# Kernel optimization log

Measured on AMD Instinct MI355X. Metric: run time of the kernel, lower is better.

## Reference

```python
import jax, jax.numpy as jnp
import numpy as np

SEQ_LEN = 4096
NUM_EIGH = 40
D_IN = 64
D_OUT = 64
K_U = 3
BSZ = 2


def _spectral_filters(L, K):
    # Hankel matrix Z_ij = 2/((i+j)^3 - (i+j)), i,j in [1, L]
    e = np.arange(1, L + 1, dtype=np.float64)
    s = e[:, None] + e[None, :]
    Z = 2.0 / (s ** 3 - s)
    sigma, phi = np.linalg.eigh(Z)
    phi_k = phi[:, -K:] * sigma[-K:] ** 0.25  # (L, K)
    return jnp.asarray(phi_k, dtype=jnp.float32)


def setup_inputs() -> dict:
    key = jax.random.key(0)
    kx, km, kp, kn = jax.random.split(key, 4)
    x = jax.random.normal(kx, (BSZ, SEQ_LEN, D_IN), dtype=jnp.float32)
    phi = _spectral_filters(SEQ_LEN, NUM_EIGH)  # (L, K)
    M = jax.random.normal(km, (D_OUT, D_IN, K_U), dtype=jnp.float32) / D_IN
    M_phi_plus = jax.random.normal(kp, (NUM_EIGH, D_IN, D_OUT), dtype=jnp.float32) / 10.0
    M_phi_minus = jax.random.normal(kn, (NUM_EIGH, D_IN, D_OUT), dtype=jnp.float32) / 10.0
    return {"x": x, "phi": phi, "M": M, "M_phi_plus": M_phi_plus, "M_phi_minus": M_phi_minus}


def _stu_forward(x, phi, M, M_phi_plus, M_phi_minus):
    bsz, L, d_in = x.shape
    n = int(2 ** np.ceil(np.log2(2 * L - 1)))  # FFT length (8192)
    t = jnp.arange(L)
    sgn = jnp.where(t % 2 == 1, -1.0, 1.0).astype(x.dtype)  # (L,)

    # FFT of [u, u*sgn] once over d_in (K-expansion deferred to freq domain; FFT is linear)
    U = jnp.stack([x, x * sgn[None, :, None]], axis=-1)        # (b, L, d, 2)
    U_f = jnp.fft.rfft(U, n=n, axis=1)                         # (b, nf, d, 2)
    v_f = jnp.fft.rfft(phi.astype(jnp.float32), n=n, axis=0)   # (nf, K)

    prod = v_f[None, :, :, None, None] * U_f[:, :, None, :, :]  # (b, nf, K, d, 2)
    U_conv = jnp.fft.irfft(prod, n=n, axis=1)[:, :L]            # (b, L, K, d, 2)
    U_plus = U_conv[..., 0]
    U_minus = U_conv[..., 1] * sgn[None, :, None, None]

    # spectral tensordot: contract (K, d_in) -> d_out
    spec = (jnp.einsum('blkd,kdo->blo', U_plus, M_phi_plus)
            + jnp.einsum('blkd,kdo->blo', U_minus, M_phi_minus))

    ar = jnp.zeros((bsz, L, M.shape[0]), dtype=x.dtype)
    for i in range(M.shape[2]):  # k_u is small and fixed
        y_i = jnp.einsum('bli,oi->blo', x, M[:, :, i])
        if i > 0:
            y_i = jnp.pad(y_i[:, : L - i], ((0, 0), (i, 0), (0, 0)))
        ar = ar + y_i
    return spec + ar


def reference(x, phi, M, M_phi_plus, M_phi_minus):
    return _stu_forward(x, phi, M, M_phi_plus, M_phi_minus)
```

## Files before the change

kernel.cpp:

```cpp
#include <hip/hip_runtime.h>

typedef short bf16x8 __attribute__((ext_vector_type(8)));
typedef float f32x4 __attribute__((ext_vector_type(4)));
typedef unsigned short u16;

__device__ __forceinline__ u16 f2bf(float f) {
    unsigned u = __builtin_bit_cast(unsigned, f);
    return (u16)((u + 0x7fffu + ((u >> 16) & 1u)) >> 16);
}

__global__ void k_prep(const float* __restrict__ x, u16* __restrict__ xpad,
                       const float* __restrict__ Mp, const float* __restrict__ Mm,
                       float* __restrict__ ApT, float* __restrict__ AmT,
                       float* __restrict__ out, int* __restrict__ counter) {
    __shared__ float tp[64 * 65], tm[64 * 65];
    if (blockIdx.x < 1024) {
        int gid = blockIdx.x * 256 + threadIdx.x;
        int b   = gid >> 17;
        int rem = gid & 131071;
        int r   = rem >> 4;
        int c4  = rem & 15;
        u16 o0 = 0, o1 = 0, o2 = 0, o3 = 0;
        if (r >= 4096) {
            const f32x4 v = *(const f32x4*)(x + ((b << 12) + (r - 4096)) * 64 + c4 * 4);
            o0 = f2bf(v.x); o1 = f2bf(v.y); o2 = f2bf(v.z); o3 = f2bf(v.w);
        }
        u16* p = xpad + ((b << 13) + r) * 64 + c4 * 4;
        p[0] = o0; p[1] = o1; p[2] = o2; p[3] = o3;
    } else if (blockIdx.x < 1064) {
        const int k = blockIdx.x - 1024, tid = threadIdx.x;
        for (int f = tid; f < 4096; f += 256) {
            int d = f >> 6, o = f & 63;
            float p = Mp[k * 4096 + f], m = Mm[k * 4096 + f];
            tp[o * 65 + d] = p + m;
            tm[o * 65 + d] = p - m;
        }
        __syncthreads();
        for (int f = tid; f < 4096; f += 256) {
            int o = f >> 6, d = f & 63;
            ApT[k * 4096 + f] = tp[o * 65 + d];
            AmT[k * 4096 + f] = tm[o * 65 + d];
        }
    } else {
        const int bz = blockIdx.x - 1064;
        if (bz == 0 && threadIdx.x == 0) *counter = 0;
        float* po = out + bz * 4096;
        #pragma unroll
        for (int i = 0; i < 4; ++i)
            *(f32x4*)(po + (threadIdx.x + i * 256) * 4) = (f32x4){0.f, 0.f, 0.f, 0.f};
    }
}

__global__ __launch_bounds__(256)
void k_build_w(const float* __restrict__ phi, const float* __restrict__ ApT,
               const float* __restrict__ AmT, const float* __restrict__ Mar,
               u16* __restrict__ wg) {
    const int sb = blockIdx.x;
    const int qb = blockIdx.y;
    const int s0 = sb * 64;
    const int q  = qb * 256 + threadIdx.x;
    const int o  = q >> 6, d = q & 63;

    float ap[40], am[40];
    #pragma unroll
    for (int k = 0; k < 40; ++k) { ap[k] = ApT[k * 4096 + q]; am[k] = AmT[k * 4096 + q]; }

    for (int j = 0; j < 64; j += 2) {
        const float* ph = phi + (s0 + j) * 40;
        float a0 = 0.f, a1 = 0.f, b0 = 0.f, b1 = 0.f;
        #pragma unroll
        for (int k = 0; k < 40; k += 2) { a0 += ph[k] * ap[k]; a1 += ph[k + 1] * ap[k + 1]; }
        #pragma unroll
        for (int k = 0; k < 40; k += 2) { b0 += ph[40 + k] * am[k]; b1 += ph[41 + k] * am[k + 1]; }
        float ev = a0 + a1, ov = b0 + b1;
        int s = s0 + j;
        if (s < 3)     ev += Mar[o * 192 + d * 3 + s];
        if (s + 1 < 3) ov += Mar[o * 192 + d * 3 + s + 1];
        wg[(size_t)s * 4096 + q]       = f2bf(ev);
        wg[(size_t)(s + 1) * 4096 + q] = f2bf(ov);
    }
}

__global__ __launch_bounds__(256, 2)
void k_spectral(const u16* __restrict__ xpad, const u16* __restrict__ wg,
                float* __restrict__ out, int* __restrict__ counter) {
    __shared__ __align__(16) u16 xs[2 * 191 * 64];
    __shared__ __align__(16) u16 wsm[2 * 64 * 64];
    __shared__ int sh;

    const int tid  = threadIdx.x;
    const int lane = tid & 63, w = tid >> 6;
    const int m15  = lane & 15, q4 = lane >> 4;
    const int par  = w >> 1, batch = w & 1;
    const int f0 = tid * 2, f1 = tid * 2 + 1;
    const int l0 = (((f0 >> 3) * 8) + ((f0 & 7) ^ ((f0 >> 3) & 7))) * 8;
    const int l1 = (((f1 >> 3) * 8) + ((f1 & 7) ^ ((f1 >> 3) & 7))) * 8;

    for (;;) {
        __syncthreads();
        if (tid == 0) sh = atomicAdd(counter, 1);
        __syncthreads();
        const int U = sh;
        if (U >= 1120) break;

        int mu = U, shalf = 0, slen = 64;
        if (U >= 992) { mu = 992 + ((U - 992) >> 1); shalf = (U - 992) & 1; slen = 32; }
        int g = 0;
        #pragma unroll 1
        while (g < 31 && (g + 1) * (64 - g) <= mu) ++g;
        const int rem = mu - g * (65 - g);
        const int cnt = 32 - g;
        const int col = (rem >= cnt) ? 1 : 0;
        const int J = 2 * g + col;
        const int I = g + (col ? rem - cnt : rem);
        const int t0 = I << 7, s0 = (J << 6) + (shalf << 5);
        const int nrows = 127 + slen;
        const int jmax = slen >> 1;
        const int base = 4096 + t0 - s0 - (slen - 1);

        const u16* wbase = wg + (size_t)s0 * 4096;
        bf16x8 pre[4];
        pre[0] = *(const bf16x8*)(wbase + f0 * 8);
        pre[1] = *(const bf16x8*)(wbase + f1 * 8);
        pre[2] = *(const bf16x8*)(wbase + 4096 + f0 * 8);
        pre[3] = *(const bf16x8*)(wbase + 4096 + f1 * 8);

        #pragma unroll
        for (int b = 0; b < 2; ++b) {
            #pragma unroll 1
            for (int f = tid; f < nrows * 8; f += 256) {
                int r = f >> 3, c = f & 7;
                bf16x8 v = *(const bf16x8*)(xpad + (size_t)((b << 13) + base + r) * 64 + c * 8);
                *(bf16x8*)(xs + ((b * 191 + r) * 8 + (c ^ (r & 7))) * 8) = v;
            }
        }

        f32x4 acc[8][4];
        #pragma unroll
        for (int mt = 0; mt < 8; ++mt)
            #pragma unroll
            for (int nt = 0; nt < 4; ++nt)
                acc[mt][nt] = (f32x4){0.f, 0.f, 0.f, 0.f};

        const u16* xb = xs + batch * (191 * 64);
        const u16* wpar = wsm + par * 4096;

        #pragma unroll 1
        for (int j = 0; j < jmax; ++j) {
            __syncthreads();
            *(bf16x8*)(wsm + l0)        = pre[0];
            *(bf16x8*)(wsm + l1)        = pre[1];
            *(bf16x8*)(wsm + 4096 + l0) = pre[2];
            *(bf16x8*)(wsm + 4096 + l1) = pre[3];
            __syncthreads();
            if (j < jmax - 1) {
                const u16* wp = wbase + (size_t)(2 * j + 2) * 4096;
                pre[0] = *(const bf16x8*)(wp + f0 * 8);
                pre[1] = *(const bf16x8*)(wp + f1 * 8);
                pre[2] = *(const bf16x8*)(wp + 4096 + f0 * 8);
                pre[3] = *(const bf16x8*)(wp + 4096 + f1 * 8);
            }
            const int ds = 2 * j + par;
            #pragma unroll
            for (int ks = 0; ks < 2; ++ks) {
                const int kq = ks * 4 + q4;
                bf16x8 bf[4];
                #pragma unroll
                for (int nt = 0; nt < 4; ++nt) {
                    int o = nt * 16 + m15;
                    bf[nt] = *(const bf16x8*)(wpar + (o * 8 + (kq ^ (o & 7))) * 8);
                }
                #pragma unroll
                for (int mt = 0; mt < 8; ++mt) {
                    int r = mt * 16 + m15 + (slen - 1) - ds;
                    bf16x8 av = *(const bf16x8*)(xb + (r * 8 + (kq ^ (r & 7))) * 8);
                    #pragma unroll
                    for (int nt = 0; nt < 4; ++nt)
                        acc[mt][nt] = __builtin_amdgcn_mfma_f32_16x16x32_bf16(
                            av, bf[nt], acc[mt][nt], 0, 0, 0);
                }
            }
        }

        float* fs = (float*)wsm;
        #pragma unroll
        for (int rd = 0; rd < 4; ++rd) {
            __syncthreads();
            if (par == 1) {
                #pragma unroll
                for (int i = 0; i < 8; ++i) {
                    int ti = rd * 8 + i;
                    *(f32x4*)(fs + (batch * 8 + i) * 256 + lane * 4) = acc[ti >> 2][ti & 3];
                }
            }
            __syncthreads();
            if (par == 0) {
                #pragma unroll
                for (int i = 0; i < 8; ++i) {
                    int ti = rd * 8 + i;
                    f32x4 v = *(const f32x4*)(fs + (batch * 8 + i) * 256 + lane * 4);
                    acc[ti >> 2][ti & 3] += v;
                }
            }
        }

        if (par == 0) {
            #pragma unroll
            for (int mt = 0; mt < 8; ++mt) {
                int t = t0 + mt * 16 + q4 * 4;
                #pragma unroll
                for (int nt = 0; nt < 4; ++nt) {
                    int o = nt * 16 + m15;
                    float* op = out + (size_t)((batch << 12) + t) * 64 + o;
                    #pragma unroll
                    for (int r = 0; r < 4; ++r)
                        atomicAdd(op + r * 64, acc[mt][nt][r]);
                }
            }
        }
    }
}

extern "C" void kernel_launch(void* const* d_in, const int* in_sizes, int n_in,
                              void* d_out, int out_size, void* d_ws, size_t ws_size,
                              hipStream_t stream) {
    const float* x   = (const float*)d_in[0];
    const float* phi = (const float*)d_in[1];
    const float* M   = (const float*)d_in[2];
    const float* Mp  = (const float*)d_in[3];
    const float* Mm  = (const float*)d_in[4];
    float* out = (float*)d_out;

    int* counter = (int*)d_ws;
    u16* xpad = (u16*)((char*)d_ws + 4096);
    u16* wg   = (u16*)((char*)d_ws + 4096 + 2097152);
    float* ApT = (float*)((char*)d_ws + 4096 + 2097152 + 33554432);
    float* AmT = ApT + 40 * 4096;

    k_prep<<<1192, 256, 0, stream>>>(x, xpad, Mp, Mm, ApT, AmT, out, counter);
    k_build_w<<<dim3(64, 16), 256, 0, stream>>>(phi, ApT, AmT, M, wg);
    k_spectral<<<512, 256, 0, stream>>>(xpad, wg, out, counter);
}
```

Before: 236.8 us.

## Restructure spectral MFMA loop to reuse A fragments across shifted filter tiles

The spectral kernel's inner loop is restructured. Warps now split the 64-wide d_in contraction into halves (khalf) instead of splitting the shift parity. Each iteration loads 4 (or 2) weight tiles spaced 16 shifts apart into enlarged shared memory, and the A fragments from the x rows are loaded into registers once and reused across those tiles via a sliding register window. This cuts repeated LDS reads of x and halves the number of barrier-separated iterations. In exchange it uses more LDS and registers, which could pressure occupancy under launch_bounds(256,2).

```diff
diff --git a/kernel.cpp b/kernel.cpp
--- a/kernel.cpp
+++ b/kernel.cpp
@@ -81,17 +81,79 @@
     }
 }
 
+
+template<int SLEN>
+__device__ __forceinline__ void run_tiles(const u16* __restrict__ wg,
+                                          const u16* xb, u16* wsm,
+                                          int s0, int kq, int m15,
+                                          int l0, int l1, int f0, int f1,
+                                          f32x4 (&acc)[8][4]) {
+    constexpr int G = SLEN / 16;
+    bf16x8 pre[G][2];
+    #pragma unroll
+    for (int t = 0; t < G; ++t) {
+        const u16* wp = wg + (size_t)(s0 + 16 * t) * 4096;
+        pre[t][0] = *(const bf16x8*)(wp + f0 * 8);
+        pre[t][1] = *(const bf16x8*)(wp + f1 * 8);
+    }
+    #pragma unroll 1
+    for (int dl = 0; dl < 16; ++dl) {
+        __syncthreads();
+        #pragma unroll
+        for (int t = 0; t < G; ++t) {
+            *(bf16x8*)(wsm + t * 4096 + l0) = pre[t][0];
+            *(bf16x8*)(wsm + t * 4096 + l1) = pre[t][1];
+        }
+        bf16x8 af[8 + G - 1];
+        const int rbase = m15 + (SLEN - 1) - dl;
+        #pragma unroll
+        for (int sg = 0; sg < 8; ++sg) {
+            int r = rbase + 16 * sg;
+            af[(G - 1) + sg] = *(const bf16x8*)(xb + (r * 8 + (kq ^ (r & 7))) * 8);
+        }
+        __syncthreads();
+        if (dl < 15) {
+            #pragma unroll
+            for (int t = 0; t < G; ++t) {
+                const u16* wp = wg + (size_t)(s0 + dl + 1 + 16 * t) * 4096;
+                pre[t][0] = *(const bf16x8*)(wp + f0 * 8);
+                pre[t][1] = *(const bf16x8*)(wp + f1 * 8);
+            }
+        }
+        #pragma unroll
+        for (int g = 0; g < G; ++g) {
+            if (g > 0) {
+                int r = rbase - 16 * g;
+                af[(G - 1) - g] = *(const bf16x8*)(xb + (r * 8 + (kq ^ (r & 7))) * 8);
+            }
+            bf16x8 bf[4];
+            #pragma unroll
+            for (int nt = 0; nt < 4; ++nt) {
+                int o = nt * 16 + m15;
+                bf[nt] = *(const bf16x8*)(wsm + g * 4096 + (o * 8 + (kq ^ (o & 7))) * 8);
+            }
+            #pragma unroll
+            for (int mt = 0; mt < 8; ++mt)
+                #pragma unroll
+                for (int nt = 0; nt < 4; ++nt)
+                    acc[mt][nt] = __builtin_amdgcn_mfma_f32_16x16x32_bf16(
+                        af[(G - 1) + mt - g], bf[nt], acc[mt][nt], 0, 0, 0);
+        }
+    }
+}
+
 __global__ __launch_bounds__(256, 2)
 void k_spectral(const u16* __restrict__ xpad, const u16* __restrict__ wg,
                 float* __restrict__ out, int* __restrict__ counter) {
     __shared__ __align__(16) u16 xs[2 * 191 * 64];
-    __shared__ __align__(16) u16 wsm[2 * 64 * 64];
+    __shared__ __align__(16) u16 wsm[4 * 64 * 64];
     __shared__ int sh;
 
     const int tid  = threadIdx.x;
     const int lane = tid & 63, w = tid >> 6;
     const int m15  = lane & 15, q4 = lane >> 4;
-    const int par  = w >> 1, batch = w & 1;
+    const int khalf = w >> 1, batch = w & 1;
+    const int kq = khalf * 4 + q4;
     const int f0 = tid * 2, f1 = tid * 2 + 1;
     const int l0 = (((f0 >> 3) * 8) + ((f0 & 7) ^ ((f0 >> 3) & 7))) * 8;
     const int l1 = (((f1 >> 3) * 8) + ((f1 & 7) ^ ((f1 >> 3) & 7))) * 8;
@@ -115,15 +177,7 @@
         const int I = g + (col ? rem - cnt : rem);
         const int t0 = I << 7, s0 = (J << 6) + (shalf << 5);
         const int nrows = 127 + slen;
-        const int jmax = slen >> 1;
         const int base = 4096 + t0 - s0 - (slen - 1);
-
-        const u16* wbase = wg + (size_t)s0 * 4096;
-        bf16x8 pre[4];
-        pre[0] = *(const bf16x8*)(wbase + f0 * 8);
-        pre[1] = *(const bf16x8*)(wbase + f1 * 8);
-        pre[2] = *(const bf16x8*)(wbase + 4096 + f0 * 8);
-        pre[3] = *(const bf16x8*)(wbase + 4096 + f1 * 8);
 
         #pragma unroll
         for (int b = 0; b < 2; ++b) {
@@ -143,50 +197,17 @@
                 acc[mt][nt] = (f32x4){0.f, 0.f, 0.f, 0.f};
 
         const u16* xb = xs + batch * (191 * 64);
-        const u16* wpar = wsm + par * 4096;
-
-        #pragma unroll 1
-        for (int j = 0; j < jmax; ++j) {
-            __syncthreads();
-            *(bf16x8*)(wsm + l0)        = pre[0];
-            *(bf16x8*)(wsm + l1)        = pre[1];
-            *(bf16x8*)(wsm + 4096 + l0) = pre[2];
-            *(bf16x8*)(wsm + 4096 + l1) = pre[3];
-            __syncthreads();
-            if (j < jmax - 1) {
-                const u16* wp = wbase + (size_t)(2 * j + 2) * 4096;
-                pre[0] = *(const bf16x8*)(wp + f0 * 8);
-                pre[1] = *(const bf16x8*)(wp + f1 * 8);
-                pre[2] = *(const bf16x8*)(wp + 4096 + f0 * 8);
-                pre[3] = *(const bf16x8*)(wp + 4096 + f1 * 8);
-            }
-            const int ds = 2 * j + par;
-            #pragma unroll
-            for (int ks = 0; ks < 2; ++ks) {
-                const int kq = ks * 4 + q4;
-                bf16x8 bf[4];
-                #pragma unroll
-                for (int nt = 0; nt < 4; ++nt) {
-                    int o = nt * 16 + m15;
-                    bf[nt] = *(const bf16x8*)(wpar + (o * 8 + (kq ^ (o & 7))) * 8);
-                }
-                #pragma unroll
-                for (int mt = 0; mt < 8; ++mt) {
-                    int r = mt * 16 + m15 + (slen - 1) - ds;
-                    bf16x8 av = *(const bf16x8*)(xb + (r * 8 + (kq ^ (r & 7))) * 8);
-                    #pragma unroll
-                    for (int nt = 0; nt < 4; ++nt)
-                        acc[mt][nt] = __builtin_amdgcn_mfma_f32_16x16x32_bf16(
-                            av, bf[nt], acc[mt][nt], 0, 0, 0);
-                }
-            }
-        }
+
+        if (slen == 64)
+            run_tiles<64>(wg, xb, wsm, s0, kq, m15, l0, l1, f0, f1, acc);
+        else
+            run_tiles<32>(wg, xb, wsm, s0, kq, m15, l0, l1, f0, f1, acc);
 
         float* fs = (float*)wsm;
         #pragma unroll
         for (int rd = 0; rd < 4; ++rd) {
             __syncthreads();
-            if (par == 1) {
+            if (khalf == 1) {
                 #pragma unroll
                 for (int i = 0; i < 8; ++i) {
                     int ti = rd * 8 + i;
@@ -194,7 +215,7 @@
                 }
             }
             __syncthreads();
-            if (par == 0) {
+            if (khalf == 0) {
                 #pragma unroll
                 for (int i = 0; i < 8; ++i) {
                     int ti = rd * 8 + i;
@@ -204,7 +225,7 @@
             }
         }
 
-        if (par == 0) {
+        if (khalf == 0) {
             #pragma unroll
             for (int mt = 0; mt < 8; ++mt) {
                 int t = t0 + mt * 16 + q4 * 4;
```

Result: slower. 255.5 us (+7.9%).

## Fuse prep and weight-build kernels, double-buffer spectral weight tiles

Applied to the files above, without the earlier changes.

Merges the prep and filter-weight build kernels into one launch. The build blocks now compute (Mp±Mm) directly from the original layout instead of going through an intermediate transposed buffer, and stage phi rows in shared memory for vectorized reads. In the spectral kernel the weight tile in LDS is double-buffered, which removes one barrier per iteration. This raises LDS use per block, and the untransposed loads of Mp/Mm are strided, so they coalesce poorly.

```diff
diff --git a/kernel.cpp b/kernel.cpp
--- a/kernel.cpp
+++ b/kernel.cpp
@@ -9,11 +9,13 @@
     return (u16)((u + 0x7fffu + ((u >> 16) & 1u)) >> 16);
 }
 
-__global__ void k_prep(const float* __restrict__ x, u16* __restrict__ xpad,
-                       const float* __restrict__ Mp, const float* __restrict__ Mm,
-                       float* __restrict__ ApT, float* __restrict__ AmT,
-                       float* __restrict__ out, int* __restrict__ counter) {
-    __shared__ float tp[64 * 65], tm[64 * 65];
+__global__ __launch_bounds__(256)
+void k_prepbuild(const float* __restrict__ x, u16* __restrict__ xpad,
+                 const float* __restrict__ phi,
+                 const float* __restrict__ Mp, const float* __restrict__ Mm,
+                 const float* __restrict__ Mar, u16* __restrict__ wg,
+                 float* __restrict__ out, int* __restrict__ counter) {
+    __shared__ __align__(16) float phis[32 * 40];
     if (blockIdx.x < 1024) {
         int gid = blockIdx.x * 256 + threadIdx.x;
         int b   = gid >> 17;
@@ -27,57 +29,47 @@
         }
         u16* p = xpad + ((b << 13) + r) * 64 + c4 * 4;
         p[0] = o0; p[1] = o1; p[2] = o2; p[3] = o3;
-    } else if (blockIdx.x < 1064) {
-        const int k = blockIdx.x - 1024, tid = threadIdx.x;
-        for (int f = tid; f < 4096; f += 256) {
-            int d = f >> 6, o = f & 63;
-            float p = Mp[k * 4096 + f], m = Mm[k * 4096 + f];
-            tp[o * 65 + d] = p + m;
-            tm[o * 65 + d] = p - m;
-        }
-        __syncthreads();
-        for (int f = tid; f < 4096; f += 256) {
-            int o = f >> 6, d = f & 63;
-            ApT[k * 4096 + f] = tp[o * 65 + d];
-            AmT[k * 4096 + f] = tm[o * 65 + d];
-        }
-    } else {
-        const int bz = blockIdx.x - 1064;
+    } else if (blockIdx.x < 1152) {
+        const int bz = blockIdx.x - 1024;
         if (bz == 0 && threadIdx.x == 0) *counter = 0;
         float* po = out + bz * 4096;
         #pragma unroll
         for (int i = 0; i < 4; ++i)
             *(f32x4*)(po + (threadIdx.x + i * 256) * 4) = (f32x4){0.f, 0.f, 0.f, 0.f};
-    }
-}
-
-__global__ __launch_bounds__(256)
-void k_build_w(const float* __restrict__ phi, const float* __restrict__ ApT,
-               const float* __restrict__ AmT, const float* __restrict__ Mar,
-               u16* __restrict__ wg) {
-    const int sb = blockIdx.x;
-    const int qb = blockIdx.y;
-    const int s0 = sb * 64;
-    const int q  = qb * 256 + threadIdx.x;
-    const int o  = q >> 6, d = q & 63;
-
-    float ap[40], am[40];
-    #pragma unroll
-    for (int k = 0; k < 40; ++k) { ap[k] = ApT[k * 4096 + q]; am[k] = AmT[k * 4096 + q]; }
-
-    for (int j = 0; j < 64; j += 2) {
-        const float* ph = phi + (s0 + j) * 40;
-        float a0 = 0.f, a1 = 0.f, b0 = 0.f, b1 = 0.f;
-        #pragma unroll
-        for (int k = 0; k < 40; k += 2) { a0 += ph[k] * ap[k]; a1 += ph[k + 1] * ap[k + 1]; }
-        #pragma unroll
-        for (int k = 0; k < 40; k += 2) { b0 += ph[40 + k] * am[k]; b1 += ph[41 + k] * am[k + 1]; }
-        float ev = a0 + a1, ov = b0 + b1;
-        int s = s0 + j;
-        if (s < 3)     ev += Mar[o * 192 + d * 3 + s];
-        if (s + 1 < 3) ov += Mar[o * 192 + d * 3 + s + 1];
-        wg[(size_t)s * 4096 + q]       = f2bf(ev);
-        wg[(size_t)(s + 1) * 4096 + q] = f2bf(ov);
+    } else {
+        const int bi = blockIdx.x - 1152;
+        const int sb = bi >> 4, qb = bi & 15;
+        const int s0 = sb * 32;
+        const int q  = qb * 256 + threadIdx.x;
+        const int o  = q >> 6, d = q & 63;
+
+        for (int f = threadIdx.x; f < 1280; f += 256) phis[f] = phi[s0 * 40 + f];
+
+        float ap[40], am[40];
+        #pragma unroll
+        for (int k = 0; k < 40; ++k) {
+            float p = Mp[k * 4096 + d * 64 + o];
+            float m = Mm[k * 4096 + d * 64 + o];
+            ap[k] = p + m; am[k] = p - m;
+        }
+        __syncthreads();
+
+        for (int j = 0; j < 32; j += 2) {
+            const float* ph = phis + j * 40;
+            float ev = 0.f, ov = 0.f;
+            #pragma unroll
+            for (int k = 0; k < 40; k += 4) {
+                f32x4 p0 = *(const f32x4*)(ph + k);
+                f32x4 p1 = *(const f32x4*)(ph + 40 + k);
+                ev += p0.x * ap[k] + p0.y * ap[k + 1] + p0.z * ap[k + 2] + p0.w * ap[k + 3];
+                ov += p1.x * am[k] + p1.y * am[k + 1] + p1.z * am[k + 2] + p1.w * am[k + 3];
+            }
+            int s = s0 + j;
+            if (s < 3)     ev += Mar[o * 192 + d * 3 + s];
+            if (s + 1 < 3) ov += Mar[o * 192 + d * 3 + s + 1];
+            wg[(size_t)s * 4096 + q]       = f2bf(ev);
+            wg[(size_t)(s + 1) * 4096 + q] = f2bf(ov);
+        }
     }
 }
 
@@ -85,7 +77,7 @@
 void k_spectral(const u16* __restrict__ xpad, const u16* __restrict__ wg,
                 float* __restrict__ out, int* __restrict__ counter) {
     __shared__ __align__(16) u16 xs[2 * 191 * 64];
-    __shared__ __align__(16) u16 wsm[2 * 64 * 64];
+    __shared__ __align__(16) u16 wsm[4 * 64 * 64];
     __shared__ int sh;
 
     const int tid  = threadIdx.x;
@@ -143,15 +135,14 @@
                 acc[mt][nt] = (f32x4){0.f, 0.f, 0.f, 0.f};
 
         const u16* xb = xs + batch * (191 * 64);
-        const u16* wpar = wsm + par * 4096;
 
         #pragma unroll 1
         for (int j = 0; j < jmax; ++j) {
-            __syncthreads();
-            *(bf16x8*)(wsm + l0)        = pre[0];
-            *(bf16x8*)(wsm + l1)        = pre[1];
-            *(bf16x8*)(wsm + 4096 + l0) = pre[2];
-            *(bf16x8*)(wsm + 4096 + l1) = pre[3];
+            u16* wdst = wsm + (j & 1) * 8192;
+            *(bf16x8*)(wdst + l0)        = pre[0];
+            *(bf16x8*)(wdst + l1)        = pre[1];
+            *(bf16x8*)(wdst + 4096 + l0) = pre[2];
+            *(bf16x8*)(wdst + 4096 + l1) = pre[3];
             __syncthreads();
             if (j < jmax - 1) {
                 const u16* wp = wbase + (size_t)(2 * j + 2) * 4096;
@@ -160,6 +151,7 @@
                 pre[2] = *(const bf16x8*)(wp + 4096 + f0 * 8);
                 pre[3] = *(const bf16x8*)(wp + 4096 + f1 * 8);
             }
+            const u16* wpar = wsm + (j & 1) * 8192 + par * 4096;
             const int ds = 2 * j + par;
             #pragma unroll
             for (int ks = 0; ks < 2; ++ks) {
@@ -234,10 +226,7 @@
     int* counter = (int*)d_ws;
     u16* xpad = (u16*)((char*)d_ws + 4096);
     u16* wg   = (u16*)((char*)d_ws + 4096 + 2097152);
-    float* ApT = (float*)((char*)d_ws + 4096 + 2097152 + 33554432);
-    float* AmT = ApT + 40 * 4096;
-
-    k_prep<<<1192, 256, 0, stream>>>(x, xpad, Mp, Mm, ApT, AmT, out, counter);
-    k_build_w<<<dim3(64, 16), 256, 0, stream>>>(phi, ApT, AmT, M, wg);
+
+    k_prepbuild<<<3200, 256, 0, stream>>>(x, xpad, phi, Mp, Mm, M, wg, out, counter);
     k_spectral<<<512, 256, 0, stream>>>(xpad, wg, out, counter);
 }
```

Measured after the change: 339.1 us. +43.2%, slower.

## Fuse prep, filter build and spectral GEMM into one persistent kernel with flag dependencies

Applied to the files above, without the earlier changes.

Merges the three launches into a single persistent kernel. Blocks take work units from an atomic queue: weight transpose, bf16 padding of x, output zeroing, per-slab filter construction, then spectral MFMA tiles. Spin-waits on completion counters enforce dependencies, so each spectral tile waits only for its own W slab. The intent is to remove launch gaps and let filter building overlap with spectral compute, at the cost of spin-wait stalls, a memset for the control words, and relying on forward progress of the atomic-ordered queue.

```diff
diff --git a/kernel.cpp b/kernel.cpp
--- a/kernel.cpp
+++ b/kernel.cpp
@@ -9,84 +9,27 @@
     return (u16)((u + 0x7fffu + ((u >> 16) & 1u)) >> 16);
 }
 
-__global__ void k_prep(const float* __restrict__ x, u16* __restrict__ xpad,
-                       const float* __restrict__ Mp, const float* __restrict__ Mm,
-                       float* __restrict__ ApT, float* __restrict__ AmT,
-                       float* __restrict__ out, int* __restrict__ counter) {
-    __shared__ float tp[64 * 65], tm[64 * 65];
-    if (blockIdx.x < 1024) {
-        int gid = blockIdx.x * 256 + threadIdx.x;
-        int b   = gid >> 17;
-        int rem = gid & 131071;
-        int r   = rem >> 4;
-        int c4  = rem & 15;
-        u16 o0 = 0, o1 = 0, o2 = 0, o3 = 0;
-        if (r >= 4096) {
-            const f32x4 v = *(const f32x4*)(x + ((b << 12) + (r - 4096)) * 64 + c4 * 4);
-            o0 = f2bf(v.x); o1 = f2bf(v.y); o2 = f2bf(v.z); o3 = f2bf(v.w);
-        }
-        u16* p = xpad + ((b << 13) + r) * 64 + c4 * 4;
-        p[0] = o0; p[1] = o1; p[2] = o2; p[3] = o3;
-    } else if (blockIdx.x < 1064) {
-        const int k = blockIdx.x - 1024, tid = threadIdx.x;
-        for (int f = tid; f < 4096; f += 256) {
-            int d = f >> 6, o = f & 63;
-            float p = Mp[k * 4096 + f], m = Mm[k * 4096 + f];
-            tp[o * 65 + d] = p + m;
-            tm[o * 65 + d] = p - m;
-        }
-        __syncthreads();
-        for (int f = tid; f < 4096; f += 256) {
-            int o = f >> 6, d = f & 63;
-            ApT[k * 4096 + f] = tp[o * 65 + d];
-            AmT[k * 4096 + f] = tm[o * 65 + d];
-        }
-    } else {
-        const int bz = blockIdx.x - 1064;
-        if (bz == 0 && threadIdx.x == 0) *counter = 0;
-        float* po = out + bz * 4096;
-        #pragma unroll
-        for (int i = 0; i < 4; ++i)
-            *(f32x4*)(po + (threadIdx.x + i * 256) * 4) = (f32x4){0.f, 0.f, 0.f, 0.f};
-    }
-}
-
-__global__ __launch_bounds__(256)
-void k_build_w(const float* __restrict__ phi, const float* __restrict__ ApT,
-               const float* __restrict__ AmT, const float* __restrict__ Mar,
-               u16* __restrict__ wg) {
-    const int sb = blockIdx.x;
-    const int qb = blockIdx.y;
-    const int s0 = sb * 64;
-    const int q  = qb * 256 + threadIdx.x;
-    const int o  = q >> 6, d = q & 63;
-
-    float ap[40], am[40];
-    #pragma unroll
-    for (int k = 0; k < 40; ++k) { ap[k] = ApT[k * 4096 + q]; am[k] = AmT[k * 4096 + q]; }
-
-    for (int j = 0; j < 64; j += 2) {
-        const float* ph = phi + (s0 + j) * 40;
-        float a0 = 0.f, a1 = 0.f, b0 = 0.f, b1 = 0.f;
-        #pragma unroll
-        for (int k = 0; k < 40; k += 2) { a0 += ph[k] * ap[k]; a1 += ph[k + 1] * ap[k + 1]; }
-        #pragma unroll
-        for (int k = 0; k < 40; k += 2) { b0 += ph[40 + k] * am[k]; b1 += ph[41 + k] * am[k + 1]; }
-        float ev = a0 + a1, ov = b0 + b1;
-        int s = s0 + j;
-        if (s < 3)     ev += Mar[o * 192 + d * 3 + s];
-        if (s + 1 < 3) ov += Mar[o * 192 + d * 3 + s + 1];
-        wg[(size_t)s * 4096 + q]       = f2bf(ev);
-        wg[(size_t)(s + 1) * 4096 + q] = f2bf(ov);
-    }
-}
+#define U_XP   40
+#define U_ZE   296
+#define U_BU   424
+#define U_SP   1448
+#define U_END  2568
 
 __global__ __launch_bounds__(256, 2)
-void k_spectral(const u16* __restrict__ xpad, const u16* __restrict__ wg,
-                float* __restrict__ out, int* __restrict__ counter) {
+void k_fused(const float* __restrict__ x, const float* __restrict__ phi,
+             const float* __restrict__ Mar,
+             const float* __restrict__ Mp, const float* __restrict__ Mm,
+             u16* __restrict__ xpad, u16* __restrict__ wg,
+             float* __restrict__ ApT, float* __restrict__ AmT,
+             float* __restrict__ out, int* __restrict__ ctrl) {
     __shared__ __align__(16) u16 xs[2 * 191 * 64];
     __shared__ __align__(16) u16 wsm[2 * 64 * 64];
     __shared__ int sh;
+
+    int* unitc  = ctrl;
+    int* tdone  = ctrl + 1;
+    int* p0done = ctrl + 2;
+    int* jdone  = ctrl + 4;
 
     const int tid  = threadIdx.x;
     const int lane = tid & 63, w = tid >> 6;
@@ -96,125 +39,232 @@
     const int l0 = (((f0 >> 3) * 8) + ((f0 & 7) ^ ((f0 >> 3) & 7))) * 8;
     const int l1 = (((f1 >> 3) * 8) + ((f1 & 7) ^ ((f1 >> 3) & 7))) * 8;
 
+    bool seen_t = false, seen_p0 = false;
+
     for (;;) {
         __syncthreads();
-        if (tid == 0) sh = atomicAdd(counter, 1);
+        if (tid == 0) sh = atomicAdd(unitc, 1);
         __syncthreads();
         const int U = sh;
-        if (U >= 1120) break;
-
-        int mu = U, shalf = 0, slen = 64;
-        if (U >= 992) { mu = 992 + ((U - 992) >> 1); shalf = (U - 992) & 1; slen = 32; }
-        int g = 0;
-        #pragma unroll 1
-        while (g < 31 && (g + 1) * (64 - g) <= mu) ++g;
-        const int rem = mu - g * (65 - g);
-        const int cnt = 32 - g;
-        const int col = (rem >= cnt) ? 1 : 0;
-        const int J = 2 * g + col;
-        const int I = g + (col ? rem - cnt : rem);
-        const int t0 = I << 7, s0 = (J << 6) + (shalf << 5);
-        const int nrows = 127 + slen;
-        const int jmax = slen >> 1;
-        const int base = 4096 + t0 - s0 - (slen - 1);
-
-        const u16* wbase = wg + (size_t)s0 * 4096;
-        bf16x8 pre[4];
-        pre[0] = *(const bf16x8*)(wbase + f0 * 8);
-        pre[1] = *(const bf16x8*)(wbase + f1 * 8);
-        pre[2] = *(const bf16x8*)(wbase + 4096 + f0 * 8);
-        pre[3] = *(const bf16x8*)(wbase + 4096 + f1 * 8);
-
-        #pragma unroll
-        for (int b = 0; b < 2; ++b) {
+        if (U >= U_END) break;
+
+        if (U < U_XP) {
+            float* tp = (float*)xs;
+            float* tm = tp + 64 * 65;
+            const int k = U;
+            for (int f = tid; f < 4096; f += 256) {
+                int d = f >> 6, o = f & 63;
+                float p = Mp[k * 4096 + f], m = Mm[k * 4096 + f];
+                tp[o * 65 + d] = p + m;
+                tm[o * 65 + d] = p - m;
+            }
+            __syncthreads();
+            for (int f = tid; f < 4096; f += 256) {
+                int o = f >> 6, d = f & 63;
+                ApT[k * 4096 + f] = tp[o * 65 + d];
+                AmT[k * 4096 + f] = tm[o * 65 + d];
+            }
+            __syncthreads();
+            if (tid == 0) {
+                __threadfence();
+                __hip_atomic_fetch_add(tdone, 1, __ATOMIC_RELEASE, __HIP_MEMORY_SCOPE_AGENT);
+            }
+        } else if (U < U_ZE) {
+            const int u = U - U_XP;
+            #pragma unroll
+            for (int i = 0; i < 4; ++i) {
+                int gid = (u * 4 + i) * 256 + tid;
+                int b = gid >> 17, rem = gid & 131071;
+                int r = rem >> 4, c4 = rem & 15;
+                u16 o0 = 0, o1 = 0, o2 = 0, o3 = 0;
+                if (r >= 4096) {
+                    const f32x4 v = *(const f32x4*)(x + ((b << 12) + (r - 4096)) * 64 + c4 * 4);
+                    o0 = f2bf(v.x); o1 = f2bf(v.y); o2 = f2bf(v.z); o3 = f2bf(v.w);
+                }
+                u16* p = xpad + ((b << 13) + r) * 64 + c4 * 4;
+                p[0] = o0; p[1] = o1; p[2] = o2; p[3] = o3;
+            }
+            __syncthreads();
+            if (tid == 0) {
+                __threadfence();
+                __hip_atomic_fetch_add(p0done, 1, __ATOMIC_RELEASE, __HIP_MEMORY_SCOPE_AGENT);
+            }
+        } else if (U < U_BU) {
+            float* po = out + (U - U_ZE) * 4096;
+            #pragma unroll
+            for (int i = 0; i < 4; ++i)
+                *(f32x4*)(po + (tid + i * 256) * 4) = (f32x4){0.f, 0.f, 0.f, 0.f};
+            __syncthreads();
+            if (tid == 0) {
+                __threadfence();
+                __hip_atomic_fetch_add(p0done, 1, __ATOMIC_RELEASE, __HIP_MEMORY_SCOPE_AGENT);
+            }
+        } else if (U < U_SP) {
+            if (!seen_t) {
+                if (tid == 0)
+                    while (__hip_atomic_load(tdone, __ATOMIC_ACQUIRE, __HIP_MEMORY_SCOPE_AGENT) < 40)
+                        __builtin_amdgcn_s_sleep(2);
+                __syncthreads();
+                seen_t = true;
+            }
+            const int v = U - U_BU;
+            const int Jg = v >> 4, qb = v & 15;
+            const int s0 = Jg * 64;
+            const int q  = qb * 256 + tid;
+            const int o  = q >> 6, d = q & 63;
+
+            float ap[40], am[40];
+            #pragma unroll
+            for (int k = 0; k < 40; ++k) {
+                ap[k] = ApT[k * 4096 + q];
+                am[k] = AmT[k * 4096 + q];
+            }
+            for (int j = 0; j < 64; j += 2) {
+                const float* ph = phi + (s0 + j) * 40;
+                float a0 = 0.f, a1 = 0.f, b0 = 0.f, b1 = 0.f;
+                #pragma unroll
+                for (int k = 0; k < 40; k += 2) { a0 += ph[k] * ap[k]; a1 += ph[k + 1] * ap[k + 1]; }
+                #pragma unroll
+                for (int k = 0; k < 40; k += 2) { b0 += ph[40 + k] * am[k]; b1 += ph[41 + k] * am[k + 1]; }
+                float ev = a0 + a1, ov = b0 + b1;
+                int s = s0 + j;
+                if (s < 3)     ev += Mar[o * 192 + d * 3 + s];
+                if (s + 1 < 3) ov += Mar[o * 192 + d * 3 + s + 1];
+                wg[(size_t)s * 4096 + q]       = f2bf(ev);
+                wg[(size_t)(s + 1) * 4096 + q] = f2bf(ov);
+            }
+            __syncthreads();
+            if (tid == 0) {
+                __threadfence();
+                __hip_atomic_fetch_add(&jdone[Jg], 1, __ATOMIC_RELEASE, __HIP_MEMORY_SCOPE_AGENT);
+            }
+        } else {
+            if (!seen_p0) {
+                if (tid == 0)
+                    while (__hip_atomic_load(p0done, __ATOMIC_ACQUIRE, __HIP_MEMORY_SCOPE_AGENT) < 384)
+                        __builtin_amdgcn_s_sleep(2);
+                __syncthreads();
+                seen_p0 = true;
+            }
+            const int su = U - U_SP;
+            int mu = su, shalf = 0, slen = 64;
+            if (su >= 992) { mu = 992 + ((su - 992) >> 1); shalf = (su - 992) & 1; slen = 32; }
+            int g = 0;
             #pragma unroll 1
-            for (int f = tid; f < nrows * 8; f += 256) {
-                int r = f >> 3, c = f & 7;
-                bf16x8 v = *(const bf16x8*)(xpad + (size_t)((b << 13) + base + r) * 64 + c * 8);
-                *(bf16x8*)(xs + ((b * 191 + r) * 8 + (c ^ (r & 7))) * 8) = v;
-            }
-        }
-
-        f32x4 acc[8][4];
-        #pragma unroll
-        for (int mt = 0; mt < 8; ++mt)
-            #pragma unroll
-            for (int nt = 0; nt < 4; ++nt)
-                acc[mt][nt] = (f32x4){0.f, 0.f, 0.f, 0.f};
-
-        const u16* xb = xs + batch * (191 * 64);
-        const u16* wpar = wsm + par * 4096;
-
-        #pragma unroll 1
-        for (int j = 0; j < jmax; ++j) {
-            __syncthreads();
-            *(bf16x8*)(wsm + l0)        = pre[0];
-            *(bf16x8*)(wsm + l1)        = pre[1];
-            *(bf16x8*)(wsm + 4096 + l0) = pre[2];
-            *(bf16x8*)(wsm + 4096 + l1) = pre[3];
-            __syncthreads();
-            if (j < jmax - 1) {
-                const u16* wp = wbase + (size_t)(2 * j + 2) * 4096;
-                pre[0] = *(const bf16x8*)(wp + f0 * 8);
-                pre[1] = *(const bf16x8*)(wp + f1 * 8);
-                pre[2] = *(const bf16x8*)(wp + 4096 + f0 * 8);
-                pre[3] = *(const bf16x8*)(wp + 4096 + f1 * 8);
-            }
-            const int ds = 2 * j + par;
-            #pragma unroll
-            for (int ks = 0; ks < 2; ++ks) {
-                const int kq = ks * 4 + q4;
-                bf16x8 bf[4];
-                #pragma unroll
-                for (int nt = 0; nt < 4; ++nt) {
-                    int o = nt * 16 + m15;
-                    bf[nt] = *(const bf16x8*)(wpar + (o * 8 + (kq ^ (o & 7))) * 8);
-                }
+            while (g < 31 && (g + 1) * (64 - g) <= mu) ++g;
+            const int rem = mu - g * (65 - g);
+            const int cnt = 32 - g;
+            const int col = (rem >= cnt) ? 1 : 0;
+            const int J = 2 * g + col;
+            const int I = g + (col ? rem - cnt : rem);
+            const int t0 = I << 7, s0 = (J << 6) + (shalf << 5);
+            const int nrows = 127 + slen;
+            const int jmax = slen >> 1;
+            const int base = 4096 + t0 - s0 - (slen - 1);
+
+            if (tid == 0)
+                while (__hip_atomic_load(&jdone[J], __ATOMIC_ACQUIRE, __HIP_MEMORY_SCOPE_AGENT) < 16)
+                    __builtin_amdgcn_s_sleep(2);
+            __syncthreads();
+
+            const u16* wbase = wg + (size_t)s0 * 4096;
+            bf16x8 pre[4];
+            pre[0] = *(const bf16x8*)(wbase + f0 * 8);
+            pre[1] = *(const bf16x8*)(wbase + f1 * 8);
+            pre[2] = *(const bf16x8*)(wbase + 4096 + f0 * 8);
+            pre[3] = *(const bf16x8*)(wbase + 4096 + f1 * 8);
+
+            #pragma unroll
+            for (int b = 0; b < 2; ++b) {
+                #pragma unroll 1
+                for (int f = tid; f < nrows * 8; f += 256) {
+                    int r = f >> 3, c = f & 7;
+                    bf16x8 v = *(const bf16x8*)(xpad + (size_t)((b << 13) + base + r) * 64 + c * 8);
+                    *(bf16x8*)(xs + ((b * 191 + r) * 8 + (c ^ (r & 7))) * 8) = v;
+                }
+            }
+
+            f32x4 acc[8][4];
+            #pragma unroll
+            for (int mt = 0; mt < 8; ++mt)
+                #pragma unroll
+                for (int nt = 0; nt < 4; ++nt)
+                    acc[mt][nt] = (f32x4){0.f, 0.f, 0.f, 0.f};
+
+            const u16* xb = xs + batch * (191 * 64);
+            const u16* wpar = wsm + par * 4096;
+
+            #pragma unroll 1
+            for (int j = 0; j < jmax; ++j) {
+                __syncthreads();
+                *(bf16x8*)(wsm + l0)        = pre[0];
+                *(bf16x8*)(wsm + l1)        = pre[1];
+                *(bf16x8*)(wsm + 4096 + l0) = pre[2];
+                *(bf16x8*)(wsm + 4096 + l1) = pre[3];
+                __syncthreads();
+                if (j < jmax - 1) {
+                    const u16* wp = wbase + (size_t)(2 * j + 2) * 4096;
+                    pre[0] = *(const bf16x8*)(wp + f0 * 8);
+                    pre[1] = *(const bf16x8*)(wp + f1 * 8);
+                    pre[2] = *(const bf16x8*)(wp + 4096 + f0 * 8);
+                    pre[3] = *(const bf16x8*)(wp + 4096 + f1 * 8);
+                }
+                const int ds = 2 * j + par;
+                #pragma unroll
+                for (int ks = 0; ks < 2; ++ks) {
+                    const int kq = ks * 4 + q4;
+                    bf16x8 bfv[4];
+                    #pragma unroll
+                    for (int nt = 0; nt < 4; ++nt) {
+                        int o = nt * 16 + m15;
+                        bfv[nt] = *(const bf16x8*)(wpar + (o * 8 + (kq ^ (o & 7))) * 8);
+                    }
+                    #pragma unroll
+                    for (int mt = 0; mt < 8; ++mt) {
+                        int r = mt * 16 + m15 + (slen - 1) - ds;
+                        bf16x8 av = *(const bf16x8*)(xb + (r * 8 + (kq ^ (r & 7))) * 8);
+                        #pragma unroll
+                        for (int nt = 0; nt < 4; ++nt)
+                            acc[mt][nt] = __builtin_amdgcn_mfma_f32_16x16x32_bf16(
+                                av, bfv[nt], acc[mt][nt], 0, 0, 0);
+                    }
+                }
+            }
+
+            float* fs = (float*)wsm;
+            #pragma unroll
+            for (int rd = 0; rd < 4; ++rd) {
+                __syncthreads();
+                if (par == 1) {
+                    #pragma unroll
+                    for (int i = 0; i < 8; ++i) {
+                        int ti = rd * 8 + i;
+                        *(f32x4*)(fs + (batch * 8 + i) * 256 + lane * 4) = acc[ti >> 2][ti & 3];
+                    }
+                }
+                __syncthreads();
+                if (par == 0) {
+                    #pragma unroll
+                    for (int i = 0; i < 8; ++i) {
+                        int ti = rd * 8 + i;
+                        f32x4 v = *(const f32x4*)(fs + (batch * 8 + i) * 256 + lane * 4);
+                        acc[ti >> 2][ti & 3] += v;
+                    }
+                }
+            }
+
+            if (par == 0) {
                 #pragma unroll
                 for (int mt = 0; mt < 8; ++mt) {
-                    int r = mt * 16 + m15 + (slen - 1) - ds;
-                    bf16x8 av = *(const bf16x8*)(xb + (r * 8 + (kq ^ (r & 7))) * 8);
-                    #pragma unroll
-                    for (int nt = 0; nt < 4; ++nt)
-                        acc[mt][nt] = __builtin_amdgcn_mfma_f32_16x16x32_bf16(
-                            av, bf[nt], acc[mt][nt], 0, 0, 0);
-                }
-            }
-        }
-
-        float* fs = (float*)wsm;
-        #pragma unroll
-        for (int rd = 0; rd < 4; ++rd) {
-            __syncthreads();
-            if (par == 1) {
-                #pragma unroll
-                for (int i = 0; i < 8; ++i) {
-                    int ti = rd * 8 + i;
-                    *(f32x4*)(fs + (batch * 8 + i) * 256 + lane * 4) = acc[ti >> 2][ti & 3];
-                }
-            }
-            __syncthreads();
-            if (par == 0) {
-                #pragma unroll
-                for (int i = 0; i < 8; ++i) {
-                    int ti = rd * 8 + i;
-                    f32x4 v = *(const f32x4*)(fs + (batch * 8 + i) * 256 + lane * 4);
-                    acc[ti >> 2][ti & 3] += v;
-                }
-            }
-        }
-
-        if (par == 0) {
-            #pragma unroll
-            for (int mt = 0; mt < 8; ++mt) {
-                int t = t0 + mt * 16 + q4 * 4;
-                #pragma unroll
-                for (int nt = 0; nt < 4; ++nt) {
-                    int o = nt * 16 + m15;
-                    float* op = out + (size_t)((batch << 12) + t) * 64 + o;
-                    #pragma unroll
-                    for (int r = 0; r < 4; ++r)
-                        atomicAdd(op + r * 64, acc[mt][nt][r]);
+                    int t = t0 + mt * 16 + q4 * 4;
+                    #pragma unroll
+                    for (int nt = 0; nt < 4; ++nt) {
+                        int o = nt * 16 + m15;
+                        float* op = out + (size_t)((batch << 12) + t) * 64 + o;
+                        #pragma unroll
+                        for (int r = 0; r < 4; ++r)
+                            atomicAdd(op + r * 64, acc[mt][nt][r]);
+                    }
                 }
             }
         }
@@ -231,13 +281,12 @@
     const float* Mm  = (const float*)d_in[4];
     float* out = (float*)d_out;
 
-    int* counter = (int*)d_ws;
+    int* ctrl = (int*)d_ws;
     u16* xpad = (u16*)((char*)d_ws + 4096);
     u16* wg   = (u16*)((char*)d_ws + 4096 + 2097152);
     float* ApT = (float*)((char*)d_ws + 4096 + 2097152 + 33554432);
     float* AmT = ApT + 40 * 4096;
 
-    k_prep<<<1192, 256, 0, stream>>>(x, xpad, Mp, Mm, ApT, AmT, out, counter);
-    k_build_w<<<dim3(64, 16), 256, 0, stream>>>(phi, ApT, AmT, M, wg);
-    k_spectral<<<512, 256, 0, stream>>>(xpad, wg, out, counter);
+    hipMemsetAsync(d_ws, 0, 4096, stream);
+    k_fused<<<512, 256, 0, stream>>>(x, phi, M, Mp, Mm, xpad, wg, ApT, AmT, out, ctrl);
 }
```

After: 351.1 us. 48.3% more time.
